# Kernel tuning notes

Measured on AMD Instinct MI355X. Metric: run time of the kernel, lower is better.

The kernel has to match this reference:

```python
import jax, jax.numpy as jnp
import numpy as np

B, S, D, H = 2, 2048, 1024, 16
HD = D // H  # per-head dim = 64


def setup_inputs() -> dict:
    key = jax.random.key(0)
    ks = jax.random.split(key, 9)
    s = 0.02
    return {
        "h": jax.random.normal(ks[0], (B, S, D), jnp.float32),
        "Wq": jax.random.normal(ks[1], (D, D), jnp.float32) * s,
        "bq": jax.random.normal(ks[2], (D,), jnp.float32) * s,
        "Wk": jax.random.normal(ks[3], (D, D), jnp.float32) * s,
        "bk": jax.random.normal(ks[4], (D,), jnp.float32) * s,
        "Wv": jax.random.normal(ks[5], (D, D), jnp.float32) * s,
        "bv": jax.random.normal(ks[6], (D,), jnp.float32) * s,
        "Wo": jax.random.normal(ks[7], (D, D), jnp.float32) * s,
        "bo": jax.random.normal(ks[8], (D,), jnp.float32) * s,
    }


def reference(h, Wq, bq, Wk, bk, Wv, bv, Wo, bo):
    b, s, d = h.shape
    # Linear projections (torch Linear: x @ W.T + b), split heads -> [B,H,S,HD]
    def split_heads(x):
        return x.reshape(b, s, H, HD).transpose(0, 2, 1, 3)

    q = split_heads(h @ Wq.T + bq)
    k = split_heads(h @ Wk.T + bk)
    v = split_heads(h @ Wv.T + bv)

    # scaled scores [B,H,S,S]
    qk = jnp.einsum("bhqd,bhkd->bhqk", q, k) / np.sqrt(HD).astype(np.float32)
    # causal mask: strictly upper triangle -> -inf
    causal = jnp.triu(jnp.ones((s, s), dtype=bool), k=1)
    qk = jnp.where(causal[None, None], -jnp.inf, qk)

    probs = jax.nn.softmax(qk, axis=-1)
    o = jnp.einsum("bhqk,bhkd->bhqd", probs, v)
    o = o.transpose(0, 2, 1, 3).reshape(b, s, d)
    return o @ Wo.T + bo
```

## Files before the change

### kernel.cpp

```cpp
#include <hip/hip_runtime.h>
#include <stdint.h>

typedef __bf16 bf16;
typedef __bf16 bf16x4_t __attribute__((ext_vector_type(4)));
typedef __bf16 bf16x8_t __attribute__((ext_vector_type(8)));
typedef float f32x4 __attribute__((ext_vector_type(4)));

static constexpr int NB = 2, SS = 2048, DD = 1024, NH = 16, HD = 64;

__device__ __forceinline__ void gl_lds16(const void* g, void* l) {
    __builtin_amdgcn_global_load_lds((__attribute__((address_space(1))) void*)g,
                                     (__attribute__((address_space(3))) void*)l, 16, 0, 0);
}

__global__ __launch_bounds__(256) void cast_all(const float* __restrict__ h,
                                                const float* __restrict__ Wq,
                                                const float* __restrict__ Wk,
                                                const float* __restrict__ Wv,
                                                const float* __restrict__ Wo,
                                                bf16* __restrict__ dst) {
    int i = blockIdx.x * 256 + threadIdx.x;
    const float* src;
    int off;
    if (i < 1048576) { src = h; off = i; }
    else {
        int r = i - 1048576;
        int w = r >> 18;
        off = r & 262143;
        src = (w == 0) ? Wq : (w == 1) ? Wk : (w == 2) ? Wv : Wo;
    }
    float4 v = reinterpret_cast<const float4*>(src)[off];
    bf16x4_t o;
    o.x = (bf16)v.x; o.y = (bf16)v.y; o.z = (bf16)v.z; o.w = (bf16)v.w;
    reinterpret_cast<bf16x4_t*>(dst)[i] = o;
}

__device__ __forceinline__ void gemm128_mainloop(const bf16* __restrict__ Ablk,
                                                 const bf16* __restrict__ Bblk,
                                                 int K, f32x4 acc[4][4]) {
    __shared__ __align__(16) bf16 As[128 * 32];
    __shared__ __align__(16) bf16 Bs[128 * 32];
    const int tid = threadIdx.x;
    const int wave = tid >> 6, lane = tid & 63;
    const int quad = lane >> 4, l15 = lane & 15;
    const int wm = wave >> 1, wn = wave & 1;

#pragma unroll
    for (int mi = 0; mi < 4; mi++)
#pragma unroll
        for (int ni = 0; ni < 4; ni++) {
            acc[mi][ni][0] = 0.f; acc[mi][ni][1] = 0.f;
            acc[mi][ni][2] = 0.f; acc[mi][ni][3] = 0.f;
        }

    const int n0c = tid;
    const int r0 = n0c >> 2, c0 = (n0c & 3) ^ ((r0 >> 1) & 3);
    const int n1c = 256 + tid;
    const int r1 = n1c >> 2, c1 = (n1c & 3) ^ ((r1 >> 1) & 3);

    for (int kk = 0; kk < K; kk += 32) {
        __syncthreads();
        gl_lds16(Ablk + (size_t)r0 * K + kk + c0 * 8, &As[(wave * 64) * 8]);
        gl_lds16(Ablk + (size_t)r1 * K + kk + c1 * 8, &As[(256 + wave * 64) * 8]);
        gl_lds16(Bblk + (size_t)r0 * K + kk + c0 * 8, &Bs[(wave * 64) * 8]);
        gl_lds16(Bblk + (size_t)r1 * K + kk + c1 * 8, &Bs[(256 + wave * 64) * 8]);
        __syncthreads();

        bf16x8_t a[4], b[4];
#pragma unroll
        for (int mi = 0; mi < 4; mi++) {
            int R = wm * 64 + mi * 16 + l15;
            a[mi] = *(const bf16x8_t*)&As[R * 32 + ((quad ^ ((R >> 1) & 3)) << 3)];
        }
#pragma unroll
        for (int ni = 0; ni < 4; ni++) {
            int R = wn * 64 + ni * 16 + l15;
            b[ni] = *(const bf16x8_t*)&Bs[R * 32 + ((quad ^ ((R >> 1) & 3)) << 3)];
        }
#pragma unroll
        for (int mi = 0; mi < 4; mi++)
#pragma unroll
            for (int ni = 0; ni < 4; ni++)
                acc[mi][ni] = __builtin_amdgcn_mfma_f32_16x16x32_bf16(a[mi], b[ni], acc[mi][ni], 0, 0, 0);
    }
}

__global__ __launch_bounds__(256) void gemm_qkv(const bf16* __restrict__ A, const bf16* __restrict__ Wqkv,
                                                const float* __restrict__ bq, const float* __restrict__ bk,
                                                const float* __restrict__ bv,
                                                bf16* __restrict__ Qb, bf16* __restrict__ Kb, bf16* __restrict__ Vb) {
    const int m0 = blockIdx.x * 128;
    const int n0 = blockIdx.y * 128;
    f32x4 acc[4][4];
    gemm128_mainloop(A + (size_t)m0 * DD, Wqkv + (size_t)n0 * DD, DD, acc);

    const int tid = threadIdx.x, wave = tid >> 6, lane = tid & 63;
    const int quad = lane >> 4, l15 = lane & 15;
    const int wm = wave >> 1, wn = wave & 1;

    const int which = n0 >> 10;
    const float* bias = (which == 0) ? bq : (which == 1) ? bk : bv;
    const float sc = (which == 0) ? 0.18033688f : 1.0f;

    const int cbase = (n0 & 1023) + wn * 64;
    const int head = cbase >> 6;
    const int bb = m0 >> 11;
    const int s0 = (m0 & 2047) + wm * 64;

    if (which == 2) {
        bf16* dbase = Vb + ((size_t)(bb * NH + head)) * HD * SS;
#pragma unroll
        for (int ni = 0; ni < 4; ni++) {
            float bsv = bias[cbase + ni * 16 + l15];
            int hd = ni * 16 + l15;
#pragma unroll
            for (int mi = 0; mi < 4; mi++) {
                bf16x4_t pb;
                pb.x = (bf16)(acc[mi][ni][0] + bsv);
                pb.y = (bf16)(acc[mi][ni][1] + bsv);
                pb.z = (bf16)(acc[mi][ni][2] + bsv);
                pb.w = (bf16)(acc[mi][ni][3] + bsv);
                int s = s0 + mi * 16 + quad * 4;
                *(bf16x4_t*)&dbase[(size_t)hd * SS + s] = pb;
            }
        }
    } else {
        bf16* dst = (which == 0) ? Qb : Kb;
        bf16* dbase = dst + ((size_t)(bb * NH + head)) * SS * HD;
#pragma unroll
        for (int ni = 0; ni < 4; ni++) {
            float bsv = bias[cbase + ni * 16 + l15];
            int hd = ni * 16 + l15;
#pragma unroll
            for (int mi = 0; mi < 4; mi++) {
#pragma unroll
                for (int r = 0; r < 4; r++) {
                    int s = s0 + mi * 16 + quad * 4 + r;
                    dbase[(size_t)s * HD + hd] = (bf16)((acc[mi][ni][r] + bsv) * sc);
                }
            }
        }
    }
}

__global__ __launch_bounds__(256) void gemm_out(const bf16* __restrict__ A, const bf16* __restrict__ Wo,
                                                const float* __restrict__ bo, float* __restrict__ out,
                                                const bf16* __restrict__ Opart, const float* __restrict__ Ml) {
    __shared__ __align__(16) bf16 As[64 * 32];
    __shared__ __align__(16) bf16 Bs[128 * 32];
    const int m0 = blockIdx.x * 64, n0 = blockIdx.y * 128;
    const int tid = threadIdx.x;
    const int wave = tid >> 6, lane = tid & 63;
    const int quad = lane >> 4, l15 = lane & 15;
    const int wm = wave >> 1, wn = wave & 1;

    f32x4 acc[2][4];
#pragma unroll
    for (int mi = 0; mi < 2; mi++)
#pragma unroll
        for (int ni = 0; ni < 4; ni++) {
            acc[mi][ni][0] = 0.f; acc[mi][ni][1] = 0.f;
            acc[mi][ni][2] = 0.f; acc[mi][ni][3] = 0.f;
        }

    const int ra = tid >> 2, ca = (tid & 3) ^ ((ra >> 1) & 3);
    const int n1c = 256 + tid;
    const int r1 = n1c >> 2, c1 = (n1c & 3) ^ ((r1 >> 1) & 3);

    const bf16* Ablk = A + (size_t)m0 * DD;
    const bf16* Bblk = Wo + (size_t)n0 * DD;

    const bool split = (m0 & 2047) >= 1024;
    const int row128 = (m0 + ra) & 127;
    const int pbase = 2 * (((m0 >> 11) * 128) + (((m0 & 2047) >> 7) - 8));

    for (int kk = 0; kk < DD; kk += 32) {
        __syncthreads();
        if (!split) {
            gl_lds16(Ablk + (size_t)ra * DD + kk + ca * 8, &As[(wave * 64) * 8]);
        } else {
            int col = kk + ca * 8;
            int hh = col >> 6, hd0 = col & 63;
            int p0 = pbase + 16 * hh;
            float m0v = Ml[p0 * 256 + row128],       l0v = Ml[p0 * 256 + 128 + row128];
            float m1v = Ml[(p0 + 1) * 256 + row128], l1v = Ml[(p0 + 1) * 256 + 128 + row128];
            bf16x8_t a0 = *(const bf16x8_t*)&Opart[(size_t)p0 * 8192 + row128 * 64 + hd0];
            bf16x8_t a1 = *(const bf16x8_t*)&Opart[(size_t)(p0 + 1) * 8192 + row128 * 64 + hd0];
            float M = fmaxf(m0v, m1v);
            float w0 = exp2f(m0v - M), w1 = exp2f(m1v - M);
            float inv = 1.f / (l0v * w0 + l1v * w1);
            w0 *= inv; w1 *= inv;
            bf16x8_t r;
#pragma unroll
            for (int j = 0; j < 8; j++)
                r[j] = (bf16)((float)a0[j] * w0 + (float)a1[j] * w1);
            *(bf16x8_t*)&As[tid * 8] = r;
        }
        gl_lds16(Bblk + (size_t)ra * DD + kk + ca * 8, &Bs[(wave * 64) * 8]);
        gl_lds16(Bblk + (size_t)r1 * DD + kk + c1 * 8, &Bs[(256 + wave * 64) * 8]);
        __syncthreads();

        bf16x8_t a[2], b[4];
#pragma unroll
        for (int mi = 0; mi < 2; mi++) {
            int R = wm * 32 + mi * 16 + l15;
            a[mi] = *(const bf16x8_t*)&As[R * 32 + ((quad ^ ((R >> 1) & 3)) << 3)];
        }
#pragma unroll
        for (int ni = 0; ni < 4; ni++) {
            int R = wn * 64 + ni * 16 + l15;
            b[ni] = *(const bf16x8_t*)&Bs[R * 32 + ((quad ^ ((R >> 1) & 3)) << 3)];
        }
#pragma unroll
        for (int mi = 0; mi < 2; mi++)
#pragma unroll
            for (int ni = 0; ni < 4; ni++)
                acc[mi][ni] = __builtin_amdgcn_mfma_f32_16x16x32_bf16(a[mi], b[ni], acc[mi][ni], 0, 0, 0);
    }

    float* obase = out + (size_t)(m0 + wm * 32) * DD + n0 + wn * 64;
#pragma unroll
    for (int ni = 0; ni < 4; ni++) {
        float bias = bo[n0 + wn * 64 + ni * 16 + l15];
#pragma unroll
        for (int mi = 0; mi < 2; mi++)
#pragma unroll
            for (int r = 0; r < 4; r++)
                obase[(size_t)(mi * 16 + quad * 4 + r) * DD + ni * 16 + l15] = acc[mi][ni][r] + bias;
    }
}

__global__ __launch_bounds__(256, 3) void attn_kernel(const bf16* __restrict__ Qb, const bf16* __restrict__ Kb,
                                                      const bf16* __restrict__ Vb, bf16* __restrict__ Ob,
                                                      bf16* __restrict__ Opart, float* __restrict__ Ml) {
    constexpr int PQ[24]  = {15,14,13,12,11,10, 9, 8, 15, 7, 14, 6, 13, 5, 12, 4, 11, 3, 10, 2,  9, 1,  8, 0};
    constexpr int PJ0[24] = { 0, 0, 0, 0, 0, 0, 0, 0,  8, 0,  8, 0,  8, 0,  8, 0,  8, 0,  8, 0,  8, 0,  8, 0};
    constexpr int PJ1[24] = { 8, 8, 8, 8, 8, 8, 8, 8, 16, 8, 15, 7, 14, 6, 13, 5, 12, 4, 11, 3, 10, 2,  9, 1};

    __shared__ __align__(16) bf16 Kt[2][64 * 64];
    __shared__ __align__(16) bf16 Vt[2][64 * 64];
    __shared__ __align__(16) bf16 Pt[4 * 32 * 64];

    const int tid = threadIdx.x, wave = tid >> 6, lane = tid & 63;
    const int quad = lane >> 4, l15 = lane & 15;
    const int bx = blockIdx.x;
    const int p = bx >> 5, bh = bx & 31;
    const int qtile = PQ[p], jbeg = PJ0[p], jend = PJ1[p];
    const bool diagpart = (jend == qtile + 1);
    const size_t hoff = (size_t)bh * SS * HD;
    const bf16* Qg = Qb + hoff + (size_t)qtile * 128 * HD;
    const bf16* Kbase = Kb + hoff;
    const bf16* Vbase = Vb + (size_t)bh * HD * SS;
    bf16* Pw = &Pt[wave * 2048];

    bf16x8_t qf[2][2];
#pragma unroll
    for (int qt = 0; qt < 2; qt++)
#pragma unroll
        for (int ks = 0; ks < 2; ks++)
            qf[qt][ks] = *(const bf16x8_t*)(Qg + (wave * 32 + qt * 16 + l15) * HD + ks * 32 + quad * 8);

    f32x4 o[2][4];
#pragma unroll
    for (int qt = 0; qt < 2; qt++)
#pragma unroll
        for (int nO = 0; nO < 4; nO++) {
            o[qt][nO][0] = 0.f; o[qt][nO][1] = 0.f; o[qt][nO][2] = 0.f; o[qt][nO][3] = 0.f;
        }
    float mrow[2] = {-__builtin_inff(), -__builtin_inff()};
    float lrow[2] = {0.f, 0.f};

    auto STAGE = [&](int j, int kh, int buf) {
        const bf16* Kg = Kbase + ((size_t)j * 128 + kh * 64) * HD;
        const bf16* Vg = Vbase + j * 128 + kh * 64;
#pragma unroll
        for (int t = 0; t < 2; t++) {
            int n = t * 256 + tid;
            int row = n >> 3, gc = (n & 7) ^ (row & 7);
            gl_lds16(Kg + row * HD + gc * 8, &Kt[buf][(t * 256 + wave * 64) * 8]);
        }
#pragma unroll
        for (int t = 0; t < 2; t++) {
            int n = t * 256 + tid;
            int row = n >> 3, gc = (n & 7) ^ (row & 7);
            gl_lds16(Vg + (size_t)row * SS + gc * 8, &Vt[buf][(t * 256 + wave * 64) * 8]);
        }
    };

    const int nHalves = (jend - jbeg) * 2;
    STAGE(jbeg, 0, 0);
    __syncthreads();
    int cur = 0;

    for (int hh = 0; hh < nHalves; hh++) {
        const int j = jbeg + (hh >> 1), kh = hh & 1;
        if (hh + 1 < nHalves) STAGE(jbeg + ((hh + 1) >> 1), (hh + 1) & 1, cur ^ 1);

        const bool diag = diagpart && (j == jend - 1);
        if (!(diag && kh == 1 && wave < 2)) {
            f32x4 st[4][2];
#pragma unroll
            for (int kt = 0; kt < 4; kt++)
#pragma unroll
                for (int qt = 0; qt < 2; qt++) {
                    st[kt][qt][0] = 0.f; st[kt][qt][1] = 0.f; st[kt][qt][2] = 0.f; st[kt][qt][3] = 0.f;
                }
            __builtin_amdgcn_s_setprio(1);
#pragma unroll
            for (int ks = 0; ks < 2; ks++) {
#pragma unroll
                for (int kt = 0; kt < 4; kt++) {
                    int R = kt * 16 + l15;
                    bf16x8_t kf = *(const bf16x8_t*)&Kt[cur][R * 64 + ((((ks << 2) | quad) ^ (R & 7)) << 3)];
#pragma unroll
                    for (int qt = 0; qt < 2; qt++)
                        st[kt][qt] = __builtin_amdgcn_mfma_f32_16x16x32_bf16(kf, qf[qt][ks], st[kt][qt], 0, 0, 0);
                }
            }
            __builtin_amdgcn_s_setprio(0);
            if (diag) {
#pragma unroll
                for (int kt = 0; kt < 4; kt++)
#pragma unroll
                    for (int qt = 0; qt < 2; qt++)
#pragma unroll
                        for (int r = 0; r < 4; r++) {
                            int key = kh * 64 + kt * 16 + quad * 4 + r;
                            int row = wave * 32 + qt * 16 + l15;
                            if (key > row) st[kt][qt][r] = -__builtin_inff();
                        }
            }

#pragma unroll
            for (int qt = 0; qt < 2; qt++) {
                float mx = -__builtin_inff();
#pragma unroll
                for (int kt = 0; kt < 4; kt++)
#pragma unroll
                    for (int r = 0; r < 4; r++) mx = fmaxf(mx, st[kt][qt][r]);
                mx = fmaxf(mx, __shfl_xor(mx, 16));
                mx = fmaxf(mx, __shfl_xor(mx, 32));
                if (!__all(mx <= mrow[qt] + 8.f)) {
                    float mnew = fmaxf(mrow[qt], mx);
                    float alpha = exp2f(mrow[qt] - mnew);
                    mrow[qt] = mnew;
                    lrow[qt] *= alpha;
#pragma unroll
                    for (int r = 0; r < 4; r++) {
                        float a = __shfl(alpha, (lane & 48) | (quad * 4 + r));
#pragma unroll
                        for (int nO = 0; nO < 4; nO++) o[qt][nO][r] *= a;
                    }
                }
                float sum = 0.f;
                const int row = qt * 16 + l15;
#pragma unroll
                for (int kt = 0; kt < 4; kt++) {
                    float p0 = exp2f(st[kt][qt][0] - mrow[qt]);
                    float p1 = exp2f(st[kt][qt][1] - mrow[qt]);
                    float p2 = exp2f(st[kt][qt][2] - mrow[qt]);
                    float p3 = exp2f(st[kt][qt][3] - mrow[qt]);
                    sum += (p0 + p1) + (p2 + p3);
                    bf16x4_t pb;
                    pb.x = (bf16)p0; pb.y = (bf16)p1; pb.z = (bf16)p2; pb.w = (bf16)p3;
                    int c = kt * 2 + (quad >> 1);
                    *(bf16x4_t*)&Pw[row * 64 + ((c ^ (row & 7)) << 3) + ((quad & 1) << 2)] = pb;
                }
                sum += __shfl_xor(sum, 16);
                sum += __shfl_xor(sum, 32);
                lrow[qt] += sum;
            }

#pragma unroll
            for (int ks = 0; ks < 2; ks++) {
                bf16x8_t pf[2];
#pragma unroll
                for (int qt = 0; qt < 2; qt++) {
                    int row = qt * 16 + l15;
                    int c = (ks << 2) | quad;
                    pf[qt] = *(const bf16x8_t*)&Pw[row * 64 + ((c ^ (row & 7)) << 3)];
                }
                __builtin_amdgcn_s_setprio(1);
#pragma unroll
                for (int nO = 0; nO < 4; nO++) {
                    int row = nO * 16 + l15;
                    int c = (ks << 2) | quad;
                    bf16x8_t vf = *(const bf16x8_t*)&Vt[cur][row * 64 + ((c ^ (row & 7)) << 3)];
#pragma unroll
                    for (int qt = 0; qt < 2; qt++)
                        o[qt][nO] = __builtin_amdgcn_mfma_f32_16x16x32_bf16(pf[qt], vf, o[qt][nO], 0, 0, 0);
                }
                __builtin_amdgcn_s_setprio(0);
            }
        }

        __syncthreads();
        cur ^= 1;
    }

    const int bb = bh >> 4, hh2 = bh & 15;
    if (qtile >= 8) {
        const int pidx = ((bh << 3) + (qtile - 8)) * 2 + (jbeg != 0 ? 1 : 0);
        bf16* Op = Opart + (size_t)pidx * (128 * 64);
        float* mlp = Ml + (size_t)pidx * 256;
#pragma unroll
        for (int qt = 0; qt < 2; qt++) {
            if (quad == 0) {
                mlp[wave * 32 + qt * 16 + l15] = mrow[qt];
                mlp[128 + wave * 32 + qt * 16 + l15] = lrow[qt];
            }
#pragma unroll
            for (int r = 0; r < 4; r++) {
                int row = wave * 32 + qt * 16 + quad * 4 + r;
#pragma unroll
                for (int nO = 0; nO < 4; nO++)
                    Op[row * 64 + nO * 16 + l15] = (bf16)o[qt][nO][r];
            }
        }
    } else {
#pragma unroll
        for (int qt = 0; qt < 2; qt++) {
#pragma unroll
            for (int r = 0; r < 4; r++) {
                float linv = 1.f / __shfl(lrow[qt], (lane & 48) | (quad * 4 + r));
                int srow = qtile * 128 + wave * 32 + qt * 16 + quad * 4 + r;
#pragma unroll
                for (int nO = 0; nO < 4; nO++)
                    Ob[((size_t)(bb * SS + srow)) * DD + hh2 * HD + nO * 16 + l15] = (bf16)(o[qt][nO][r] * linv);
            }
        }
    }
}

extern "C" void kernel_launch(void* const* d_in, const int* in_sizes, int n_in,
                              void* d_out, int out_size, void* d_ws, size_t ws_size,
                              hipStream_t stream) {
    (void)in_sizes; (void)n_in; (void)out_size; (void)ws_size;
    const float* h  = (const float*)d_in[0];
    const float* Wq = (const float*)d_in[1];
    const float* bq = (const float*)d_in[2];
    const float* Wk = (const float*)d_in[3];
    const float* bk = (const float*)d_in[4];
    const float* Wv = (const float*)d_in[5];
    const float* bv = (const float*)d_in[6];
    const float* Wo = (const float*)d_in[7];
    const float* bo = (const float*)d_in[8];
    float* out = (float*)d_out;

    char* ws = (char*)d_ws;
    bf16* hbf  = (bf16*)(ws);
    bf16* wqkv = (bf16*)(ws + 8388608);
    bf16* wo   = (bf16*)(ws + 8388608 + 6291456);
    bf16* Qb   = (bf16*)(ws + 16777216);
    bf16* Kb   = (bf16*)(ws + 16777216 + 8388608);
    bf16* Vb   = (bf16*)(ws + 16777216 + 2 * 8388608);
    bf16* Ob   = (bf16*)(ws + 16777216 + 3 * 8388608);
    bf16*  Opart = (bf16*)(ws);
    float* Ml    = (float*)(ws + 8388608);

    cast_all<<<8192, 256, 0, stream>>>(h, Wq, Wk, Wv, Wo, hbf);
    gemm_qkv<<<dim3(32, 24), 256, 0, stream>>>(hbf, wqkv, bq, bk, bv, Qb, Kb, Vb);
    attn_kernel<<<768, 256, 0, stream>>>(Qb, Kb, Vb, Ob, Opart, Ml);
    gemm_out<<<dim3(64, 8), 256, 0, stream>>>(Ob, wo, bo, out, Opart, Ml);
}
```

Before: 192.0 us.

## Enlarge out-projection tile to 128x128 and precompute split-merge weights in LDS

```diff
diff --git a/kernel.cpp b/kernel.cpp
--- a/kernel.cpp
+++ b/kernel.cpp
@@ -146,64 +146,87 @@
 __global__ __launch_bounds__(256) void gemm_out(const bf16* __restrict__ A, const bf16* __restrict__ Wo,
                                                 const float* __restrict__ bo, float* __restrict__ out,
                                                 const bf16* __restrict__ Opart, const float* __restrict__ Ml) {
-    __shared__ __align__(16) bf16 As[64 * 32];
+    __shared__ __align__(16) bf16 As[128 * 32];
     __shared__ __align__(16) bf16 Bs[128 * 32];
-    const int m0 = blockIdx.x * 64, n0 = blockIdx.y * 128;
+    __shared__ float Wt[128][32];
+
+    const int m0 = blockIdx.x * 128, n0 = blockIdx.y * 128;
     const int tid = threadIdx.x;
     const int wave = tid >> 6, lane = tid & 63;
     const int quad = lane >> 4, l15 = lane & 15;
     const int wm = wave >> 1, wn = wave & 1;
 
-    f32x4 acc[2][4];
-#pragma unroll
-    for (int mi = 0; mi < 2; mi++)
+    const bool split = (m0 & 2047) >= 1024;
+    const int pbase = 2 * ((m0 >> 11) * 128 + ((m0 & 2047) >> 7) - 8);
+
+    if (split) {
+        for (int i = tid; i < 2048; i += 256) {
+            int row = i >> 4, hh = i & 15;
+            int p0 = pbase + 16 * hh;
+            float m0v = Ml[(size_t)p0 * 256 + row],       l0v = Ml[(size_t)p0 * 256 + 128 + row];
+            float m1v = Ml[(size_t)(p0 + 1) * 256 + row], l1v = Ml[(size_t)(p0 + 1) * 256 + 128 + row];
+            float M = fmaxf(m0v, m1v);
+            float w0 = exp2f(m0v - M), w1 = exp2f(m1v - M);
+            float inv = 1.f / (l0v * w0 + l1v * w1);
+            Wt[row][hh * 2] = w0 * inv;
+            Wt[row][hh * 2 + 1] = w1 * inv;
+        }
+    }
+
+    f32x4 acc[4][4];
+#pragma unroll
+    for (int mi = 0; mi < 4; mi++)
 #pragma unroll
         for (int ni = 0; ni < 4; ni++) {
             acc[mi][ni][0] = 0.f; acc[mi][ni][1] = 0.f;
             acc[mi][ni][2] = 0.f; acc[mi][ni][3] = 0.f;
         }
 
-    const int ra = tid >> 2, ca = (tid & 3) ^ ((ra >> 1) & 3);
+    const int r0 = tid >> 2, c0 = (tid & 3) ^ ((r0 >> 1) & 3);
     const int n1c = 256 + tid;
     const int r1 = n1c >> 2, c1 = (n1c & 3) ^ ((r1 >> 1) & 3);
 
     const bf16* Ablk = A + (size_t)m0 * DD;
     const bf16* Bblk = Wo + (size_t)n0 * DD;
-
-    const bool split = (m0 & 2047) >= 1024;
-    const int row128 = (m0 + ra) & 127;
-    const int pbase = 2 * (((m0 >> 11) * 128) + (((m0 & 2047) >> 7) - 8));
 
     for (int kk = 0; kk < DD; kk += 32) {
         __syncthreads();
         if (!split) {
-            gl_lds16(Ablk + (size_t)ra * DD + kk + ca * 8, &As[(wave * 64) * 8]);
+            gl_lds16(Ablk + (size_t)r0 * DD + kk + c0 * 8, &As[(wave * 64) * 8]);
+            gl_lds16(Ablk + (size_t)r1 * DD + kk + c1 * 8, &As[(256 + wave * 64) * 8]);
         } else {
-            int col = kk + ca * 8;
-            int hh = col >> 6, hd0 = col & 63;
-            int p0 = pbase + 16 * hh;
-            float m0v = Ml[p0 * 256 + row128],       l0v = Ml[p0 * 256 + 128 + row128];
-            float m1v = Ml[(p0 + 1) * 256 + row128], l1v = Ml[(p0 + 1) * 256 + 128 + row128];
-            bf16x8_t a0 = *(const bf16x8_t*)&Opart[(size_t)p0 * 8192 + row128 * 64 + hd0];
-            bf16x8_t a1 = *(const bf16x8_t*)&Opart[(size_t)(p0 + 1) * 8192 + row128 * 64 + hd0];
-            float M = fmaxf(m0v, m1v);
-            float w0 = exp2f(m0v - M), w1 = exp2f(m1v - M);
-            float inv = 1.f / (l0v * w0 + l1v * w1);
-            w0 *= inv; w1 *= inv;
-            bf16x8_t r;
-#pragma unroll
-            for (int j = 0; j < 8; j++)
-                r[j] = (bf16)((float)a0[j] * w0 + (float)a1[j] * w1);
-            *(bf16x8_t*)&As[tid * 8] = r;
-        }
-        gl_lds16(Bblk + (size_t)ra * DD + kk + ca * 8, &Bs[(wave * 64) * 8]);
+            const int hh = kk >> 6;
+            const int p0 = pbase + 16 * hh;
+            const size_t ob0 = (size_t)p0 * 8192, ob1 = (size_t)(p0 + 1) * 8192;
+            {
+                int hd0 = (kk & 63) + c0 * 8;
+                bf16x8_t a0 = *(const bf16x8_t*)&Opart[ob0 + r0 * 64 + hd0];
+                bf16x8_t a1 = *(const bf16x8_t*)&Opart[ob1 + r0 * 64 + hd0];
+                float w0 = Wt[r0][hh * 2], w1 = Wt[r0][hh * 2 + 1];
+                bf16x8_t r;
+#pragma unroll
+                for (int j = 0; j < 8; j++) r[j] = (bf16)((float)a0[j] * w0 + (float)a1[j] * w1);
+                *(bf16x8_t*)&As[tid * 8] = r;
+            }
+            {
+                int hd0 = (kk & 63) + c1 * 8;
+                bf16x8_t a0 = *(const bf16x8_t*)&Opart[ob0 + r1 * 64 + hd0];
+                bf16x8_t a1 = *(const bf16x8_t*)&Opart[ob1 + r1 * 64 + hd0];
+                float w0 = Wt[r1][hh * 2], w1 = Wt[r1][hh * 2 + 1];
+                bf16x8_t r;
+#pragma unroll
+                for (int j = 0; j < 8; j++) r[j] = (bf16)((float)a0[j] * w0 + (float)a1[j] * w1);
+                *(bf16x8_t*)&As[(256 + tid) * 8] = r;
+            }
+        }
+        gl_lds16(Bblk + (size_t)r0 * DD + kk + c0 * 8, &Bs[(wave * 64) * 8]);
         gl_lds16(Bblk + (size_t)r1 * DD + kk + c1 * 8, &Bs[(256 + wave * 64) * 8]);
         __syncthreads();
 
-        bf16x8_t a[2], b[4];
-#pragma unroll
-        for (int mi = 0; mi < 2; mi++) {
-            int R = wm * 32 + mi * 16 + l15;
+        bf16x8_t a[4], b[4];
+#pragma unroll
+        for (int mi = 0; mi < 4; mi++) {
+            int R = wm * 64 + mi * 16 + l15;
             a[mi] = *(const bf16x8_t*)&As[R * 32 + ((quad ^ ((R >> 1) & 3)) << 3)];
         }
 #pragma unroll
@@ -212,18 +235,18 @@
             b[ni] = *(const bf16x8_t*)&Bs[R * 32 + ((quad ^ ((R >> 1) & 3)) << 3)];
         }
 #pragma unroll
-        for (int mi = 0; mi < 2; mi++)
+        for (int mi = 0; mi < 4; mi++)
 #pragma unroll
             for (int ni = 0; ni < 4; ni++)
                 acc[mi][ni] = __builtin_amdgcn_mfma_f32_16x16x32_bf16(a[mi], b[ni], acc[mi][ni], 0, 0, 0);
     }
 
-    float* obase = out + (size_t)(m0 + wm * 32) * DD + n0 + wn * 64;
+    float* obase = out + (size_t)(m0 + wm * 64) * DD + n0 + wn * 64;
 #pragma unroll
     for (int ni = 0; ni < 4; ni++) {
         float bias = bo[n0 + wn * 64 + ni * 16 + l15];
 #pragma unroll
-        for (int mi = 0; mi < 2; mi++)
+        for (int mi = 0; mi < 4; mi++)
 #pragma unroll
             for (int r = 0; r < 4; r++)
                 obase[(size_t)(mi * 16 + quad * 4 + r) * DD + ni * 16 + l15] = acc[mi][ni][r] + bias;
@@ -461,5 +484,5 @@
     cast_all<<<8192, 256, 0, stream>>>(h, Wq, Wk, Wv, Wo, hbf);
     gemm_qkv<<<dim3(32, 24), 256, 0, stream>>>(hbf, wqkv, bq, bk, bv, Qb, Kb, Vb);
     attn_kernel<<<768, 256, 0, stream>>>(Qb, Kb, Vb, Ob, Opart, Ml);
-    gemm_out<<<dim3(64, 8), 256, 0, stream>>>(Ob, wo, bo, out, Opart, Ml);
-}
+    gemm_out<<<dim3(32, 8), 256, 0, stream>>>(Ob, wo, bo, out, Opart, Ml);
+}
```

Result: slower. 199.1 us, median of 2 (+3.7%).
